# Optimization experiments

Hardware: AMD Instinct MI355X
Metric: run time of the kernel (lower is better)

Reference implementation:

```python
import jax, jax.numpy as jnp
import numpy as np

D_MODEL = 1024
NHEAD = 16
D_K = D_MODEL // NHEAD
EPS = 1e-5


def _layernorm(x, scale, bias):
    m = jnp.mean(x, axis=-1, keepdims=True)
    v = jnp.var(x, axis=-1, keepdims=True)
    return (x - m) * jax.lax.rsqrt(v + EPS) * scale + bias


def setup_inputs() -> dict:
    key = jax.random.key(0)
    ks = jax.random.split(key, 16)
    d, h = D_MODEL, 4 * D_MODEL
    s = 1.0 / np.sqrt(d)
    inp = {
        "x": jax.random.normal(ks[0], (2, 2048, d), dtype=jnp.float32),
        "Wq": jax.random.normal(ks[1], (d, d), dtype=jnp.float32) * s,
        "bq": jnp.zeros((d,), jnp.float32),
        "Wk": jax.random.normal(ks[2], (d, d), dtype=jnp.float32) * s,
        "bk": jnp.zeros((d,), jnp.float32),
        "Wv": jax.random.normal(ks[3], (d, d), dtype=jnp.float32) * s,
        "bv": jnp.zeros((d,), jnp.float32),
        "Wo": jax.random.normal(ks[4], (d, d), dtype=jnp.float32) * s,
        "bo": jnp.zeros((d,), jnp.float32),
        "ln1_scale": jnp.ones((d,), jnp.float32),
        "ln1_bias": jnp.zeros((d,), jnp.float32),
        "ln2_scale": jnp.ones((d,), jnp.float32),
        "ln2_bias": jnp.zeros((d,), jnp.float32),
        "W1": jax.random.normal(ks[5], (d, h), dtype=jnp.float32) * s,
        "b1": jnp.zeros((h,), jnp.float32),
        "W2": jax.random.normal(ks[6], (h, d), dtype=jnp.float32) * (1.0 / np.sqrt(h)),
        "b2": jnp.zeros((d,), jnp.float32),
    }
    return inp


def reference(x, Wq, bq, Wk, bk, Wv, bv, Wo, bo,
              ln1_scale, ln1_bias, ln2_scale, ln2_bias,
              W1, b1, W2, b2):
    batch, seq, d_model = x.shape
    # Faithful to original: q is viewed WITHOUT transpose (asymmetric vs k,v)
    q = (x @ Wq + bq).reshape(batch, NHEAD, seq, D_K)
    k = (x @ Wk + bk).reshape(batch, seq, NHEAD, D_K).transpose(0, 2, 1, 3)
    v = (x @ Wv + bv).reshape(batch, seq, NHEAD, D_K).transpose(0, 2, 1, 3)
    # scores: [B, H, S, S]
    scores = jnp.einsum('bhqd,bhkd->bhqk', q, k) / np.sqrt(D_K)
    attn = jax.nn.softmax(scores, axis=-1)
    o = jnp.einsum('bhqk,bhkd->bhqd', attn, v)  # [B,H,S,dk]
    o = o.transpose(0, 2, 1, 3).reshape(batch, seq, d_model)
    x = _layernorm(x + o @ Wo + bo, ln1_scale, ln1_bias)
    ff = jax.nn.relu(x @ W1 + b1) @ W2 + b2
    x = _layernorm(x + ff, ln2_scale, ln2_bias)
    return x
```

## Files before the change

### kernel.cpp

```cpp
#include <hip/hip_runtime.h>
#include <cstdint>

typedef __bf16 bf16x8 __attribute__((ext_vector_type(8)));
typedef float  floatx4 __attribute__((ext_vector_type(4)));

__device__ __forceinline__ unsigned short f2bf(float x) {
  union { float f; uint32_t u; } v; v.f = x;
  uint32_t r = (v.u + 0x7FFFu + ((v.u >> 16) & 1u)) >> 16;
  return (unsigned short)r;
}

__device__ __forceinline__ void async_copy16(const void* g, void* l) {
  __builtin_amdgcn_global_load_lds(
      (const __attribute__((address_space(1))) uint32_t*)g,
      (__attribute__((address_space(3))) uint32_t*)l, 16, 0, 0);
}

template<int OUT_BF16, int RELU>
__global__ __launch_bounds__(256, 2)
void gemm_bt_kernel(const unsigned short* __restrict__ A,
                    const unsigned short* __restrict__ Bt,
                    void* __restrict__ C, const float* __restrict__ bias,
                    int M, int N, int K, int Kper) {
  __shared__ __align__(16) unsigned short l0A[128 * 32];
  __shared__ __align__(16) unsigned short l0B[128 * 32];
  __shared__ __align__(16) unsigned short l1A[128 * 32];
  __shared__ __align__(16) unsigned short l1B[128 * 32];
  const int tid  = threadIdx.x;
  const int wave = tid >> 6;
  const int lane = tid & 63;

  const int gx = gridDim.x, gy = gridDim.y;
  int flat = blockIdx.y * gx + blockIdx.x;
  const int per = (gx * gy) >> 3;
  flat = (flat & 7) * per + (flat >> 3);
  const int sq = flat >> 6, inner = flat & 63;
  const int sqm = gy >> 3;
  const int m0 = ((sq % sqm) * 8 + (inner & 7)) * 128;
  const int n0 = ((sq / sqm) * 8 + (inner >> 3)) * 128;

  const int kz = blockIdx.z;
  const int wm = (wave >> 1) * 64;
  const int wn = (wave & 1) * 64;
  const int sa_row = lane >> 2;
  const int sa_k   = ((lane & 3) ^ ((lane >> 3) & 3)) * 8;
  const int fr = lane & 15;
  const int fq = lane >> 4;
  const int sw = (fr >> 1) & 3;

  const int r0 = (wave * 2 + 0) * 16 + sa_row;
  const int r1 = (wave * 2 + 1) * 16 + sa_row;
  const unsigned short* A0 = A  + (size_t)(m0 + r0) * K + kz * Kper + sa_k;
  const unsigned short* A1 = A  + (size_t)(m0 + r1) * K + kz * Kper + sa_k;
  const unsigned short* B0 = Bt + (size_t)(n0 + r0) * K + kz * Kper + sa_k;
  const unsigned short* B1 = Bt + (size_t)(n0 + r1) * K + kz * Kper + sa_k;

  floatx4 acc[4][4];
  #pragma unroll
  for (int i = 0; i < 4; ++i)
    #pragma unroll
    for (int j = 0; j < 4; ++j)
      acc[i][j] = (floatx4){0.f, 0.f, 0.f, 0.f};

  const int c0 = (wave * 2 + 0) * 512;
  const int c1 = (wave * 2 + 1) * 512;

#define PREFETCH(kt, LA, LB)                                   \
  do {                                                         \
    const int koff = (kt) << 5;                                \
    async_copy16(A0 + koff, &(LA)[c0]);                        \
    async_copy16(A1 + koff, &(LA)[c1]);                        \
    async_copy16(B0 + koff, &(LB)[c0]);                        \
    async_copy16(B1 + koff, &(LB)[c1]);                        \
  } while (0)

#define COMPUTE(LA, LB)                                                        \
  do {                                                                         \
    bf16x8 af[4], bf[4];                                                       \
    _Pragma("unroll")                                                          \
    for (int t = 0; t < 4; ++t) {                                              \
      af[t] = *(const bf16x8*)&(LA)[(wm + t * 16 + fr) * 32 + (fq ^ sw) * 8];  \
      bf[t] = *(const bf16x8*)&(LB)[(wn + t * 16 + fr) * 32 + (fq ^ sw) * 8];  \
    }                                                                          \
    _Pragma("unroll")                                                          \
    for (int mt = 0; mt < 4; ++mt)                                             \
      _Pragma("unroll")                                                        \
      for (int nt = 0; nt < 4; ++nt)                                           \
        acc[mt][nt] = __builtin_amdgcn_mfma_f32_16x16x32_bf16(af[mt], bf[nt],  \
                                                              acc[mt][nt], 0, 0, 0); \
  } while (0)

  const int kIters = Kper >> 5;
  PREFETCH(0, l0A, l0B);
  for (int kt = 0; kt < kIters; kt += 2) {
    PREFETCH(kt + 1, l1A, l1B);
    asm volatile("s_waitcnt vmcnt(4)" ::: "memory");
    asm volatile("s_barrier" ::: "memory");
    COMPUTE(l0A, l0B);
    asm volatile("s_barrier" ::: "memory");
    if (kt + 2 < kIters) {
      PREFETCH(kt + 2, l0A, l0B);
      asm volatile("s_waitcnt vmcnt(4)" ::: "memory");
    } else {
      asm volatile("s_waitcnt vmcnt(0)" ::: "memory");
    }
    asm volatile("s_barrier" ::: "memory");
    COMPUTE(l1A, l1B);
    asm volatile("s_barrier" ::: "memory");
  }
#undef PREFETCH
#undef COMPUTE

  const float* bp = (kz == 0) ? bias : nullptr;
  char* Cz = (char*)C + (size_t)kz * M * N * (OUT_BF16 ? 2 : 4);
  #pragma unroll
  for (int mt = 0; mt < 4; ++mt) {
    #pragma unroll
    for (int nt = 0; nt < 4; ++nt) {
      const int gn = n0 + wn + nt * 16 + fr;
      const float bv = bp ? bp[gn] : 0.f;
      #pragma unroll
      for (int r = 0; r < 4; ++r) {
        const int gm = m0 + wm + mt * 16 + fq * 4 + r;
        float v = acc[mt][nt][r] + bv;
        if (RELU) v = fmaxf(v, 0.f);
        if (OUT_BF16) ((unsigned short*)Cz)[(size_t)gm * N + gn] = f2bf(v);
        else          ((float*)Cz)[(size_t)gm * N + gn] = v;
      }
    }
  }
}

__global__ __launch_bounds__(256)
void repack_v_kernel(const unsigned short* __restrict__ X,
                     unsigned short* __restrict__ Vt) {
  const int bid = blockIdx.x;
  const int st = bid & 31, h = (bid >> 5) & 15, b = bid >> 9;
  const int bh = b * 16 + h;
  const int s0 = st * 64;
  const int t = threadIdx.x;
  const int sl = t >> 2;
  const int c  = (t & 3) * 16;
  __shared__ __align__(16) unsigned short vt[64][72];
  {
    const uint4* srcV = (const uint4*)(X + (size_t)(b * 2048 + s0 + sl) * 3072 + 2048 + h * 64 + c);
    uint4* dstL = (uint4*)&vt[sl][c];
    dstL[0] = srcV[0]; dstL[1] = srcV[1];
  }
  __syncthreads();
  const int d = t >> 2, cc = (t & 3) * 16;
  unsigned short tmp[16];
  #pragma unroll
  for (int j = 0; j < 16; ++j) {
    const int chat = cc + j;
    const int key = (chat & 3) * 16 + (chat >> 2);
    tmp[j] = vt[key][d];
  }
  uint4* dstV = (uint4*)(Vt + ((size_t)bh * 64 + d) * 2048 + s0 + cc);
  dstV[0] = *(uint4*)&tmp[0];
  dstV[1] = *(uint4*)&tmp[8];
}

__global__ __launch_bounds__(256, 4)
void flash_attn_kernel(const unsigned short* __restrict__ QKVb,
                       const unsigned short* __restrict__ Vt,
                       float* __restrict__ Opart, float* __restrict__ Lpart) {
  const int bid = blockIdx.x;
  const int qt = bid & 15, h = (bid >> 4) & 15, b = (bid >> 8) & 1, ksp = bid >> 9;
  const int bh = b * 16 + h;
  const int wave = threadIdx.x >> 6, lane = threadIdx.x & 63;
  const int fr = lane & 15, fq = lane >> 4;

  __shared__ __align__(16) unsigned short lK[64 * 64];
  __shared__ __align__(16) unsigned short lV[64 * 64];
  __shared__ __align__(16) unsigned short lP[4][32 * 72];

  const int q_base = qt * 128 + wave * 32;
  bf16x8 aq[2][2];
  #pragma unroll
  for (int g = 0; g < 2; ++g) {
    const int s2 = q_base + g * 16 + fr;
    const unsigned short* qp = QKVb + (size_t)(b * 2048 + h * 128 + (s2 >> 4)) * 3072
                             + (s2 & 15) * 64 + fq * 8;
    aq[g][0] = *(const bf16x8*)qp;
    aq[g][1] = *(const bf16x8*)(qp + 32);
  }
  floatx4 o_acc[2][4];
  #pragma unroll
  for (int g = 0; g < 2; ++g)
    #pragma unroll
    for (int nt = 0; nt < 4; ++nt) o_acc[g][nt] = (floatx4){0.f, 0.f, 0.f, 0.f};
  float lrow[2][4];
  #pragma unroll
  for (int g = 0; g < 2; ++g)
    #pragma unroll
    for (int r = 0; r < 4; ++r) lrow[g][r] = 0.f;

  const unsigned short* Kg = QKVb + 1024 + h * 64;
  const unsigned short* Vg = Vt + (size_t)bh * 64 * 2048;

  const int srow = lane >> 3;
  const int scol = ((lane & 7) ^ (lane >> 3)) * 8;
  const int sw = fr & 7;

  for (int kt = ksp * 16; kt < ksp * 16 + 16; ++kt) {
    __syncthreads();
    #pragma unroll
    for (int j = 0; j < 2; ++j) {
      const int ch = wave * 2 + j;
      const int krow = ch * 8 + srow;
      async_copy16(Kg + (size_t)(b * 2048 + kt * 64 + krow) * 3072 + scol, (char*)lK + ch * 1024);
      async_copy16(Vg + (size_t)krow * 2048 + kt * 64 + scol, (char*)lV + ch * 1024);
    }
    asm volatile("s_waitcnt vmcnt(0)" ::: "memory");
    __syncthreads();

    floatx4 s_acc[2][4];
    #pragma unroll
    for (int nt = 0; nt < 4; ++nt) {
      const int row = (nt * 16 + fr) * 64;
      bf16x8 bk0 = *(const bf16x8*)&lK[row + ((0 + fq) ^ sw) * 8];
      bf16x8 bk1 = *(const bf16x8*)&lK[row + ((4 + fq) ^ sw) * 8];
      #pragma unroll
      for (int g = 0; g < 2; ++g) {
        floatx4 acc = (floatx4){0.f, 0.f, 0.f, 0.f};
        acc = __builtin_amdgcn_mfma_f32_16x16x32_bf16(aq[g][0], bk0, acc, 0, 0, 0);
        acc = __builtin_amdgcn_mfma_f32_16x16x32_bf16(aq[g][1], bk1, acc, 0, 0, 0);
        s_acc[g][nt] = acc;
      }
    }
    #pragma unroll
    for (int g = 0; g < 2; ++g) {
      #pragma unroll
      for (int r = 0; r < 4; ++r) {
        const float p0 = __builtin_amdgcn_exp2f(s_acc[g][0][r] * 0.18033688f);
        const float p1 = __builtin_amdgcn_exp2f(s_acc[g][1][r] * 0.18033688f);
        const float p2 = __builtin_amdgcn_exp2f(s_acc[g][2][r] * 0.18033688f);
        const float p3 = __builtin_amdgcn_exp2f(s_acc[g][3][r] * 0.18033688f);
        lrow[g][r] += (p0 + p1) + (p2 + p3);
        union { float f; uint32_t u; } c0, c1, c2, c3;
        c0.f = p0; c1.f = p1; c2.f = p2; c3.f = p3;
        uint2 pk;
        pk.x = (c1.u & 0xffff0000u) | (c0.u >> 16);
        pk.y = (c3.u & 0xffff0000u) | (c2.u >> 16);
        *(uint2*)&lP[wave][(g * 16 + fq * 4 + r) * 72 + fr * 4] = pk;
      }
    }
    #pragma unroll
    for (int g = 0; g < 2; ++g) {
      #pragma unroll
      for (int kk = 0; kk < 2; ++kk) {
        bf16x8 ap = *(const bf16x8*)&lP[wave][(g * 16 + fr) * 72 + kk * 32 + fq * 8];
        #pragma unroll
        for (int nt = 0; nt < 4; ++nt) {
          bf16x8 bv = *(const bf16x8*)&lV[(nt * 16 + fr) * 64 + ((kk * 4 + fq) ^ sw) * 8];
          o_acc[g][nt] = __builtin_amdgcn_mfma_f32_16x16x32_bf16(ap, bv, o_acc[g][nt], 0, 0, 0);
        }
      }
    }
  }

  const size_t rbase = (size_t)ksp * 65536 + (size_t)bh * 2048 + q_base;
  #pragma unroll
  for (int g = 0; g < 2; ++g) {
    #pragma unroll
    for (int r = 0; r < 4; ++r) {
      float l = lrow[g][r];
      #pragma unroll
      for (int off = 1; off < 16; off <<= 1) l += __shfl_xor(l, off);
      if (fr == 0) Lpart[rbase + g * 16 + fq * 4 + r] = l;
    }
    #pragma unroll
    for (int nt = 0; nt < 4; ++nt)
      #pragma unroll
      for (int r = 0; r < 4; ++r)
        Opart[(rbase + g * 16 + fq * 4 + r) * 64 + nt * 16 + fr] = o_acc[g][nt][r];
  }
}

__global__ __launch_bounds__(256)
void attn_combine_kernel(const float* __restrict__ Opart, const float* __restrict__ Lpart,
                         unsigned short* __restrict__ O) {
  const int i = blockIdx.x * 256 + threadIdx.x;
  const int row = i >> 4;
  const int d4 = (i & 15) * 4;
  const float4 o0 = *(const float4*)&Opart[(size_t)row * 64 + d4];
  const float4 o1 = *(const float4*)&Opart[(size_t)(row + 65536) * 64 + d4];
  const float inv = 1.f / (Lpart[row] + Lpart[row + 65536]);
  const int bq = ((row >> 15) << 11) | (row & 2047);
  const int h = (row >> 11) & 15;
  ushort4 r;
  r.x = f2bf((o0.x + o1.x) * inv);
  r.y = f2bf((o0.y + o1.y) * inv);
  r.z = f2bf((o0.z + o1.z) * inv);
  r.w = f2bf((o0.w + o1.w) * inv);
  *(ushort4*)&O[(size_t)bq * 1024 + h * 64 + d4] = r;
}

__global__ __launch_bounds__(256)
void ln_kernel(const float* __restrict__ X, const float* __restrict__ R,
               const float* __restrict__ R2,
               const float* __restrict__ sc, const float* __restrict__ bi,
               float* __restrict__ outF, unsigned short* __restrict__ outB) {
  const int row = blockIdx.x;
  const int t = threadIdx.x;
  const size_t base = (size_t)row * 1024 + t * 4;
  float4 a  = *(const float4*)&X[base];
  const float4 rv = *(const float4*)&R[base];
  const float4 r2 = *(const float4*)&R2[base];
  a.x += rv.x + r2.x; a.y += rv.y + r2.y; a.z += rv.z + r2.z; a.w += rv.w + r2.w;
  float sum = (a.x + a.y) + (a.z + a.w);
  float sq  = (a.x * a.x + a.y * a.y) + (a.z * a.z + a.w * a.w);
  #pragma unroll
  for (int off = 32; off > 0; off >>= 1) {
    sum += __shfl_down(sum, off);
    sq  += __shfl_down(sq, off);
  }
  __shared__ float s1[4], s2a[4];
  const int wave = t >> 6, lane = t & 63;
  if (lane == 0) { s1[wave] = sum; s2a[wave] = sq; }
  __syncthreads();
  sum = (s1[0] + s1[1]) + (s1[2] + s1[3]);
  sq  = (s2a[0] + s2a[1]) + (s2a[2] + s2a[3]);
  const float mean = sum * (1.f / 1024.f);
  const float var  = sq * (1.f / 1024.f) - mean * mean;
  const float rstd = rsqrtf(var + 1e-5f);
  const float4 s = *(const float4*)&sc[t * 4];
  const float4 bb = *(const float4*)&bi[t * 4];
  float4 y;
  y.x = (a.x - mean) * rstd * s.x + bb.x;
  y.y = (a.y - mean) * rstd * s.y + bb.y;
  y.z = (a.z - mean) * rstd * s.z + bb.z;
  y.w = (a.w - mean) * rstd * s.w + bb.w;
  if (outF) *(float4*)&outF[base] = y;
  if (outB) {
    ushort4 ob; ob.x = f2bf(y.x); ob.y = f2bf(y.y); ob.z = f2bf(y.z); ob.w = f2bf(y.w);
    *(ushort4*)&outB[base] = ob;
  }
}

__global__ void transpose_all_kernel(const float* __restrict__ Wq, const float* __restrict__ Wk,
                                     const float* __restrict__ Wv, const float* __restrict__ Wo,
                                     const float* __restrict__ W1, const float* __restrict__ W2,
                                     unsigned short* __restrict__ Wqkvt, unsigned short* __restrict__ Wot,
                                     unsigned short* __restrict__ W1t, unsigned short* __restrict__ W2t) {
  const int id = blockIdx.x;
  const float* W; unsigned short* Wt; int K, N, tile;
  if (id < 4096) {
    const int w = id >> 10; tile = id & 1023; K = 1024; N = 1024;
    if (w == 0)      { W = Wq; Wt = Wqkvt; }
    else if (w == 1) { W = Wk; Wt = Wqkvt + 1024 * 1024; }
    else if (w == 2) { W = Wv; Wt = Wqkvt + 2048 * 1024; }
    else             { W = Wo; Wt = Wot; }
  } else if (id < 8192) { tile = id - 4096; W = W1; Wt = W1t; K = 1024; N = 4096; }
  else                  { tile = id - 8192; W = W2; Wt = W2t; K = 4096; N = 1024; }
  const int tilesX = N >> 5;
  const int bx = (tile & (tilesX - 1)) * 32;
  const int by = (tile / tilesX) * 32;
  __shared__ float tl[32][33];
  const int tx = threadIdx.x, ty = threadIdx.y;
  #pragma unroll
  for (int i = ty; i < 32; i += 8)
    tl[i][tx] = W[(size_t)(by + i) * N + bx + tx];
  __syncthreads();
  #pragma unroll
  for (int i = ty; i < 32; i += 8)
    Wt[(size_t)(bx + i) * K + by + tx] = f2bf(tl[tx][i]);
}

__global__ void cast_bf16_kernel(const float* __restrict__ in,
                                 unsigned short* __restrict__ out, int n4) {
  const int i = blockIdx.x * 256 + threadIdx.x;
  if (i < n4) {
    float4 v = ((const float4*)in)[i];
    ushort4 o;
    o.x = f2bf(v.x); o.y = f2bf(v.y); o.z = f2bf(v.z); o.w = f2bf(v.w);
    ((ushort4*)out)[i] = o;
  }
}

__global__ void concat3_kernel(const float* __restrict__ a, const float* __restrict__ b,
                               const float* __restrict__ c, float* __restrict__ out) {
  int i = blockIdx.x * 256 + threadIdx.x;
  if (i < 1024) out[i] = a[i];
  else if (i < 2048) out[i] = b[i - 1024];
  else if (i < 3072) out[i] = c[i - 2048];
}

extern "C" void kernel_launch(void* const* d_in, const int* in_sizes, int n_in,
                              void* d_out, int out_size, void* d_ws, size_t ws_size,
                              hipStream_t stream) {
  const float* x    = (const float*)d_in[0];
  const float* Wq   = (const float*)d_in[1];
  const float* bq   = (const float*)d_in[2];
  const float* Wk   = (const float*)d_in[3];
  const float* bk   = (const float*)d_in[4];
  const float* Wv   = (const float*)d_in[5];
  const float* bv   = (const float*)d_in[6];
  const float* Wo   = (const float*)d_in[7];
  const float* bo   = (const float*)d_in[8];
  const float* ln1s = (const float*)d_in[9];
  const float* ln1b = (const float*)d_in[10];
  const float* ln2s = (const float*)d_in[11];
  const float* ln2b = (const float*)d_in[12];
  const float* W1   = (const float*)d_in[13];
  const float* b1   = (const float*)d_in[14];
  const float* W2   = (const float*)d_in[15];
  const float* b2   = (const float*)d_in[16];
  float* out = (float*)d_out;

  char* ws = (char*)d_ws;
  const size_t MB = 1u << 20;
  unsigned short* QKVb = (unsigned short*)(ws + 0);
  float*          t1   = (float*)(ws + 0);
  unsigned short* ffh  = (unsigned short*)(ws + 0);
  unsigned short* Vt   = (unsigned short*)(ws + 32 * MB);
  unsigned short* Ob   = (unsigned short*)(ws + 40 * MB);
  float*          ff   = (float*)(ws + 32 * MB);
  float*          Opart= (float*)(ws + 48 * MB);
  unsigned short* xb   = (unsigned short*)(ws + 48 * MB);
  unsigned short* Wqkvt= (unsigned short*)(ws + 56 * MB);
  float*          x1   = (float*)(ws + 64 * MB);
  float*          Lpart= (float*)(ws + 80 * MB);
  unsigned short* Wot  = (unsigned short*)(ws + 81 * MB);
  unsigned short* W1t  = (unsigned short*)(ws + 83 * MB);
  unsigned short* W2t  = (unsigned short*)(ws + 91 * MB);
  float*          bqkv = (float*)(ws + 99 * MB);
  unsigned short* x1b  = (unsigned short*)(ws + 100 * MB);

  cast_bf16_kernel<<<4096, 256, 0, stream>>>(x, xb, 1048576);
  transpose_all_kernel<<<12288, dim3(32, 8), 0, stream>>>(Wq, Wk, Wv, Wo, W1, W2,
                                                          Wqkvt, Wot, W1t, W2t);
  concat3_kernel<<<12, 256, 0, stream>>>(bq, bk, bv, bqkv);

  gemm_bt_kernel<1, 0><<<dim3(24, 32, 1), 256, 0, stream>>>(xb, Wqkvt, QKVb, bqkv, 4096, 3072, 1024, 1024);
  repack_v_kernel<<<1024, 256, 0, stream>>>(QKVb, Vt);
  flash_attn_kernel<<<1024, 256, 0, stream>>>(QKVb, Vt, Opart, Lpart);
  attn_combine_kernel<<<4096, 256, 0, stream>>>(Opart, Lpart, Ob);
  gemm_bt_kernel<0, 0><<<dim3(8, 32, 2), 256, 0, stream>>>(Ob, Wot, t1, bo, 4096, 1024, 1024, 512);
  ln_kernel<<<4096, 256, 0, stream>>>(x, t1, t1 + 4096 * 1024, ln1s, ln1b, x1, x1b);
  gemm_bt_kernel<1, 1><<<dim3(32, 32, 1), 256, 0, stream>>>(x1b, W1t, ffh, b1, 4096, 4096, 1024, 1024);
  gemm_bt_kernel<0, 0><<<dim3(8, 32, 2), 256, 0, stream>>>(ffh, W2t, ff, b2, 4096, 1024, 4096, 2048);
  ln_kernel<<<4096, 256, 0, stream>>>(x1, ff, ff + 4096 * 1024, ln2s, ln2b, out, nullptr);

  (void)in_sizes; (void)n_in; (void)out_size; (void)ws_size;
}
```

Before: 362.6 us.

## Double-buffer K/V tiles in flash attention and store partial outputs as bf16

The flash attention loop now ping-pongs between two LDS buffers for K and V. It prefetches the next tile asynchronously while computing the current one, synchronising with partial vmcnt waits and raw barriers. Partial output accumulators are written as bf16 instead of fp32, halving write and read traffic in the combine kernel, which now processes 8 elements per thread. The cost is more LDS per block, with launch bounds dropped to 3 blocks per CU, plus some extra rounding error in the partial sums.

New measurement: 365.6 us. No clear change (+0.8%).

```diff
diff --git a/kernel.cpp b/kernel.cpp
--- a/kernel.cpp
+++ b/kernel.cpp
@@ -8,6 +8,12 @@
   union { float f; uint32_t u; } v; v.f = x;
   uint32_t r = (v.u + 0x7FFFu + ((v.u >> 16) & 1u)) >> 16;
   return (unsigned short)r;
+}
+__device__ __forceinline__ float bflo(uint32_t u) {
+  union { uint32_t u; float f; } v; v.u = u << 16; return v.f;
+}
+__device__ __forceinline__ float bfhi(uint32_t u) {
+  union { uint32_t u; float f; } v; v.u = u & 0xffff0000u; return v.f;
 }
 
 __device__ __forceinline__ void async_copy16(const void* g, void* l) {
@@ -161,18 +167,20 @@
   dstV[1] = *(uint4*)&tmp[8];
 }
 
-__global__ __launch_bounds__(256, 4)
+__global__ __launch_bounds__(256, 3)
 void flash_attn_kernel(const unsigned short* __restrict__ QKVb,
                        const unsigned short* __restrict__ Vt,
-                       float* __restrict__ Opart, float* __restrict__ Lpart) {
+                       unsigned short* __restrict__ Opart, float* __restrict__ Lpart) {
   const int bid = blockIdx.x;
   const int qt = bid & 15, h = (bid >> 4) & 15, b = (bid >> 8) & 1, ksp = bid >> 9;
   const int bh = b * 16 + h;
   const int wave = threadIdx.x >> 6, lane = threadIdx.x & 63;
   const int fr = lane & 15, fq = lane >> 4;
 
-  __shared__ __align__(16) unsigned short lK[64 * 64];
-  __shared__ __align__(16) unsigned short lV[64 * 64];
+  __shared__ __align__(16) unsigned short lK0[64 * 64];
+  __shared__ __align__(16) unsigned short lV0[64 * 64];
+  __shared__ __align__(16) unsigned short lK1[64 * 64];
+  __shared__ __align__(16) unsigned short lV1[64 * 64];
   __shared__ __align__(16) unsigned short lP[4][32 * 72];
 
   const int q_base = qt * 128 + wave * 32;
@@ -202,25 +210,23 @@
   const int srow = lane >> 3;
   const int scol = ((lane & 7) ^ (lane >> 3)) * 8;
   const int sw = fr & 7;
-
-  for (int kt = ksp * 16; kt < ksp * 16 + 16; ++kt) {
-    __syncthreads();
-    #pragma unroll
-    for (int j = 0; j < 2; ++j) {
-      const int ch = wave * 2 + j;
-      const int krow = ch * 8 + srow;
-      async_copy16(Kg + (size_t)(b * 2048 + kt * 64 + krow) * 3072 + scol, (char*)lK + ch * 1024);
-      async_copy16(Vg + (size_t)krow * 2048 + kt * 64 + scol, (char*)lV + ch * 1024);
-    }
-    asm volatile("s_waitcnt vmcnt(0)" ::: "memory");
-    __syncthreads();
-
+  const int ch0 = wave * 2, ch1 = wave * 2 + 1;
+  const int krow0 = ch0 * 8 + srow, krow1 = ch1 * 8 + srow;
+
+  auto pref = [&](int kt, unsigned short* LK, unsigned short* LV) {
+    async_copy16(Kg + (size_t)(b * 2048 + kt * 64 + krow0) * 3072 + scol, (char*)LK + ch0 * 1024);
+    async_copy16(Vg + (size_t)krow0 * 2048 + kt * 64 + scol,              (char*)LV + ch0 * 1024);
+    async_copy16(Kg + (size_t)(b * 2048 + kt * 64 + krow1) * 3072 + scol, (char*)LK + ch1 * 1024);
+    async_copy16(Vg + (size_t)krow1 * 2048 + kt * 64 + scol,              (char*)LV + ch1 * 1024);
+  };
+
+  auto compute_tile = [&](const unsigned short* LK, const unsigned short* LV) {
     floatx4 s_acc[2][4];
     #pragma unroll
     for (int nt = 0; nt < 4; ++nt) {
       const int row = (nt * 16 + fr) * 64;
-      bf16x8 bk0 = *(const bf16x8*)&lK[row + ((0 + fq) ^ sw) * 8];
-      bf16x8 bk1 = *(const bf16x8*)&lK[row + ((4 + fq) ^ sw) * 8];
+      bf16x8 bk0 = *(const bf16x8*)&LK[row + ((0 + fq) ^ sw) * 8];
+      bf16x8 bk1 = *(const bf16x8*)&LK[row + ((4 + fq) ^ sw) * 8];
       #pragma unroll
       for (int g = 0; g < 2; ++g) {
         floatx4 acc = (floatx4){0.f, 0.f, 0.f, 0.f};
@@ -253,11 +259,30 @@
         bf16x8 ap = *(const bf16x8*)&lP[wave][(g * 16 + fr) * 72 + kk * 32 + fq * 8];
         #pragma unroll
         for (int nt = 0; nt < 4; ++nt) {
-          bf16x8 bv = *(const bf16x8*)&lV[(nt * 16 + fr) * 64 + ((kk * 4 + fq) ^ sw) * 8];
+          bf16x8 bv = *(const bf16x8*)&LV[(nt * 16 + fr) * 64 + ((kk * 4 + fq) ^ sw) * 8];
           o_acc[g][nt] = __builtin_amdgcn_mfma_f32_16x16x32_bf16(ap, bv, o_acc[g][nt], 0, 0, 0);
         }
       }
     }
+  };
+
+  const int kt0 = ksp * 16;
+  pref(kt0, lK0, lV0);
+  for (int kt = kt0; kt < kt0 + 16; kt += 2) {
+    pref(kt + 1, lK1, lV1);
+    asm volatile("s_waitcnt vmcnt(4)" ::: "memory");
+    asm volatile("s_barrier" ::: "memory");
+    compute_tile(lK0, lV0);
+    asm volatile("s_barrier" ::: "memory");
+    if (kt + 2 < kt0 + 16) {
+      pref(kt + 2, lK0, lV0);
+      asm volatile("s_waitcnt vmcnt(4)" ::: "memory");
+    } else {
+      asm volatile("s_waitcnt vmcnt(0)" ::: "memory");
+    }
+    asm volatile("s_barrier" ::: "memory");
+    compute_tile(lK1, lV1);
+    asm volatile("s_barrier" ::: "memory");
   }
 
   const size_t rbase = (size_t)ksp * 65536 + (size_t)bh * 2048 + q_base;
@@ -274,27 +299,34 @@
     for (int nt = 0; nt < 4; ++nt)
       #pragma unroll
       for (int r = 0; r < 4; ++r)
-        Opart[(rbase + g * 16 + fq * 4 + r) * 64 + nt * 16 + fr] = o_acc[g][nt][r];
+        Opart[(rbase + g * 16 + fq * 4 + r) * 64 + nt * 16 + fr] = f2bf(o_acc[g][nt][r]);
   }
 }
 
 __global__ __launch_bounds__(256)
-void attn_combine_kernel(const float* __restrict__ Opart, const float* __restrict__ Lpart,
+void attn_combine_kernel(const unsigned short* __restrict__ Opart,
+                         const float* __restrict__ Lpart,
                          unsigned short* __restrict__ O) {
   const int i = blockIdx.x * 256 + threadIdx.x;
-  const int row = i >> 4;
-  const int d4 = (i & 15) * 4;
-  const float4 o0 = *(const float4*)&Opart[(size_t)row * 64 + d4];
-  const float4 o1 = *(const float4*)&Opart[(size_t)(row + 65536) * 64 + d4];
+  const int row = i >> 3;
+  const int d8 = (i & 7) * 8;
+  const uint4 a = *(const uint4*)&Opart[(size_t)row * 64 + d8];
+  const uint4 c = *(const uint4*)&Opart[(size_t)(row + 65536) * 64 + d8];
   const float inv = 1.f / (Lpart[row] + Lpart[row + 65536]);
   const int bq = ((row >> 15) << 11) | (row & 2047);
   const int h = (row >> 11) & 15;
-  ushort4 r;
-  r.x = f2bf((o0.x + o1.x) * inv);
-  r.y = f2bf((o0.y + o1.y) * inv);
-  r.z = f2bf((o0.z + o1.z) * inv);
-  r.w = f2bf((o0.w + o1.w) * inv);
-  *(ushort4*)&O[(size_t)bq * 1024 + h * 64 + d4] = r;
+  uint4 o;
+  const uint32_t au[4] = {a.x, a.y, a.z, a.w};
+  const uint32_t cu[4] = {c.x, c.y, c.z, c.w};
+  uint32_t ou[4];
+  #pragma unroll
+  for (int k = 0; k < 4; ++k) {
+    const float lo = (bflo(au[k]) + bflo(cu[k])) * inv;
+    const float hi = (bfhi(au[k]) + bfhi(cu[k])) * inv;
+    ou[k] = (uint32_t)f2bf(lo) | ((uint32_t)f2bf(hi) << 16);
+  }
+  o.x = ou[0]; o.y = ou[1]; o.z = ou[2]; o.w = ou[3];
+  *(uint4*)&O[(size_t)bq * 1024 + h * 64 + d8] = o;
 }
 
 __global__ __launch_bounds__(256)
@@ -417,7 +449,7 @@
   unsigned short* Vt   = (unsigned short*)(ws + 32 * MB);
   unsigned short* Ob   = (unsigned short*)(ws + 40 * MB);
   float*          ff   = (float*)(ws + 32 * MB);
-  float*          Opart= (float*)(ws + 48 * MB);
+  unsigned short* Opart= (unsigned short*)(ws + 48 * MB);
   unsigned short* xb   = (unsigned short*)(ws + 48 * MB);
   unsigned short* Wqkvt= (unsigned short*)(ws + 56 * MB);
   float*          x1   = (float*)(ws + 64 * MB);
@@ -436,7 +468,7 @@
   gemm_bt_kernel<1, 0><<<dim3(24, 32, 1), 256, 0, stream>>>(xb, Wqkvt, QKVb, bqkv, 4096, 3072, 1024, 1024);
   repack_v_kernel<<<1024, 256, 0, stream>>>(QKVb, Vt);
   flash_attn_kernel<<<1024, 256, 0, stream>>>(QKVb, Vt, Opart, Lpart);
-  attn_combine_kernel<<<4096, 256, 0, stream>>>(Opart, Lpart, Ob);
+  attn_combine_kernel<<<2048, 256, 0, stream>>>(Opart, Lpart, Ob);
   gemm_bt_kernel<0, 0><<<dim3(8, 32, 2), 256, 0, stream>>>(Ob, Wot, t1, bo, 4096, 1024, 1024, 512);
   ln_kernel<<<4096, 256, 0, stream>>>(x, t1, t1 + 4096 * 1024, ln1s, ln1b, x1, x1b);
   gemm_bt_kernel<1, 1><<<dim3(32, 32, 1), 256, 0, stream>>>(x1b, W1t, ffh, b1, 4096, 4096, 1024, 1024);
```
